# Kernel optimization log

Measured on AMD Instinct MI355X. Metric: run time of the kernel, lower is better.

## Reference

```python
import math
import jax, jax.numpy as jnp
import numpy as np

B, C, H, W = 8, 512, 32, 32
N_HEADS = 8
N_GROUPS = 32  # GroupNorm(32) as in guided-diffusion normalization()
EPS = 1e-5


def setup_inputs() -> dict:
    key = jax.random.key(0)
    k0, k1, k2, k3, k4 = jax.random.split(key, 5)
    x = jax.random.normal(k0, (B, C, H, W), dtype=jnp.float32)
    gn_scale = jnp.ones((C,), dtype=jnp.float32)
    gn_bias = jnp.zeros((C,), dtype=jnp.float32)
    # 1x1 conv weights stored as (out, in); proj_out is zero-initialized in the
    # original but we use small random weights so the op is non-trivial.
    qkv_w = jax.random.normal(k1, (3 * C, C), dtype=jnp.float32) * 0.02
    qkv_b = jax.random.normal(k2, (3 * C,), dtype=jnp.float32) * 0.02
    proj_w = jax.random.normal(k3, (C, C), dtype=jnp.float32) * 0.02
    proj_b = jax.random.normal(k4, (C,), dtype=jnp.float32) * 0.02
    return {"x": x, "gn_scale": gn_scale, "gn_bias": gn_bias,
            "qkv_w": qkv_w, "qkv_b": qkv_b, "proj_w": proj_w, "proj_b": proj_b}


def reference(x, gn_scale, gn_bias, qkv_w, qkv_b, proj_w, proj_b):
    b, c, h, w = x.shape
    L = h * w
    xf = x.reshape(b, c, L)

    # GroupNorm(32): normalize over (channels-in-group, length)
    xg = xf.reshape(b, N_GROUPS, c // N_GROUPS, L)
    mu = jnp.mean(xg, axis=(2, 3), keepdims=True)
    var = jnp.var(xg, axis=(2, 3), keepdims=True)
    xn = ((xg - mu) * jax.lax.rsqrt(var + EPS)).reshape(b, c, L)
    xn = xn * gn_scale[None, :, None] + gn_bias[None, :, None]

    # 1x1 conv -> qkv (b, 3c, L)
    qkv = jnp.einsum('oc,bcl->bol', qkv_w, xn) + qkv_b[None, :, None]

    ch = c // N_HEADS  # head dim (width//(3*n_heads) of qkv)
    q, k, v = jnp.split(qkv, 3, axis=1)
    q = q.reshape(b * N_HEADS, ch, L)
    k = k.reshape(b * N_HEADS, ch, L)
    v = v.reshape(b * N_HEADS, ch, L)

    scale = 1.0 / math.sqrt(math.sqrt(ch))
    # scores: (b*heads, L, L) materialized, as in the original
    wts = jnp.einsum('bct,bcs->bts', q * scale, k * scale)
    wts = jax.nn.softmax(wts.astype(jnp.float32), axis=-1).astype(q.dtype)
    a = jnp.einsum('bts,bcs->bct', wts, v).reshape(b, c, L)

    # zero-initialized 1x1 proj in original; random weights here
    hout = jnp.einsum('oc,bcl->bol', proj_w, a) + proj_b[None, :, None]
    return (xf + hout).reshape(b, c, h, w)
```

## Files before the change

kernel.cpp:

```cpp
#include <hip/hip_runtime.h>
#include <math.h>

#define BATCH   8
#define CCH     512
#define LL      1024
#define NHEADS  8
#define CHD     64
#define EPSV    1e-5f
#define QSCALE  0.1803368801111204f

typedef __bf16 bf16_t;
typedef bf16_t bf16x8 __attribute__((ext_vector_type(8)));
typedef bf16_t bf16x4 __attribute__((ext_vector_type(4)));
typedef float  f32x4  __attribute__((ext_vector_type(4)));

__device__ __forceinline__ bf16_t f2b(float f) {
  unsigned u = __float_as_uint(f);
  u += 0x7fff + ((u >> 16) & 1);
  return __builtin_bit_cast(bf16_t, (unsigned short)(u >> 16));
}

__device__ __forceinline__ unsigned pack2(float lo, float hi) {
  unsigned a = (unsigned)__builtin_bit_cast(unsigned short, f2b(lo));
  unsigned b = (unsigned)__builtin_bit_cast(unsigned short, f2b(hi));
  return (b << 16) | a;
}

__device__ __forceinline__ void gload_lds16(const void* g, void* l) {
  __builtin_amdgcn_global_load_lds(
      (const __attribute__((address_space(1))) void*)g,
      (__attribute__((address_space(3))) void*)l, 16, 0, 0);
}

__global__ __launch_bounds__(256) void prep_fused(const float* __restrict__ qkvw,
                                                  const float* __restrict__ projw,
                                                  bf16_t* __restrict__ wqb,
                                                  bf16_t* __restrict__ wpb,
                                                  const float* __restrict__ x,
                                                  const float* __restrict__ gsc,
                                                  const float* __restrict__ gbi,
                                                  bf16_t* __restrict__ xnT) {
  int bid = blockIdx.x;
  int tid = threadIdx.x;
  if (bid < 1024) {
    int i = (bid * 256 + tid) * 4;
    const float* src;
    bf16_t* dst;
    int j;
    if (i < 1536 * 512) { src = qkvw; dst = wqb; j = i; }
    else                { src = projw; dst = wpb; j = i - 1536 * 512; }
    float4 v = *(const float4*)(src + j);
    bf16x4 o = {f2b(v.x), f2b(v.y), f2b(v.z), f2b(v.w)};
    *(bf16x4*)(dst + j) = o;
    return;
  }
  int lin = bid - 1024;
  int xcd = lin & 7, slot = lin >> 3;
  int b = slot & 7, jj = slot >> 3;
  int g = xcd * 4 + jj;
  const float4* x4 = (const float4*)(x + ((size_t)(b * 32 + g)) * 16 * LL);

  float s = 0.f, ss = 0.f;
  float4 v[16];
#pragma unroll
  for (int it = 0; it < 16; ++it) {
    float4 f = x4[it * 256 + tid];
    v[it] = f;
    s += f.x + f.y + f.z + f.w;
    ss += f.x * f.x + f.y * f.y + f.z * f.z + f.w * f.w;
  }
#pragma unroll
  for (int m = 1; m < 64; m <<= 1) { s += __shfl_xor(s, m); ss += __shfl_xor(ss, m); }
  __shared__ float rs_[4], rss[4];
  int wv = tid >> 6, ln = tid & 63;
  if (ln == 0) { rs_[wv] = s; rss[wv] = ss; }
  __syncthreads();
  s  = rs_[0] + rs_[1] + rs_[2] + rs_[3];
  ss = rss[0] + rss[1] + rss[2] + rss[3];
  float mean = s * (1.f / 16384.f);
  float var  = ss * (1.f / 16384.f) - mean * mean;
  float rstd = rsqrtf(var + EPSV);

  float sc[16], bi[16];
#pragma unroll
  for (int it = 0; it < 16; ++it) {
    sc[it] = gsc[g * 16 + it] * rstd;
    bi[it] = gbi[g * 16 + it] - mean * sc[it];
  }

#pragma unroll
  for (int j = 0; j < 4; ++j) {
    unsigned w[8];
#pragma unroll
    for (int k = 0; k < 8; ++k) {
      float a0 = (j == 0 ? v[2 * k].x : j == 1 ? v[2 * k].y : j == 2 ? v[2 * k].z : v[2 * k].w);
      float a1 = (j == 0 ? v[2 * k + 1].x : j == 1 ? v[2 * k + 1].y : j == 2 ? v[2 * k + 1].z : v[2 * k + 1].w);
      w[k] = pack2(a0 * sc[2 * k] + bi[2 * k], a1 * sc[2 * k + 1] + bi[2 * k + 1]);
    }
    int l = tid * 4 + j;
    bf16_t* dst = xnT + ((size_t)b * LL + l) * CCH + g * 16;
    *(uint4*)dst = make_uint4(w[0], w[1], w[2], w[3]);
    *(uint4*)(dst + 8) = make_uint4(w[4], w[5], w[6], w[7]);
  }
}

__global__ __launch_bounds__(256, 3) void qkv_mfma(const bf16_t* __restrict__ wq,
                                                   const bf16_t* __restrict__ xnT,
                                                   const float* __restrict__ qkvb,
                                                   bf16_t* __restrict__ qt,
                                                   bf16_t* __restrict__ kt,
                                                   bf16_t* __restrict__ vt) {
  __shared__ bf16_t As[128 * 64];
  __shared__ bf16_t Bs[2][128 * 64];
  int tid = threadIdx.x;
  int wave = tid >> 6, lane = tid & 63;
  int lrow = lane & 15, quad = lane >> 4;
  int wm = wave >> 1, wn = wave & 1;
  int b = blockIdx.x;
  int oBase = blockIdx.y * 128, lBase = blockIdx.z * 128;
  int srow = lane >> 3;
  int sgOff = (((lane & 7) ^ srow) << 4);

#pragma unroll
  for (int j = 0; j < 4; ++j) {
    int ci = wave * 4 + j;
    int R = ci * 8 + srow;
    gload_lds16((const char*)(xnT + ((size_t)b * LL + lBase + R) * CCH) + sgOff,
                (char*)&Bs[0][0] + ci * 1024);
  }

  f32x4 acc[4][4] = {};
  for (int ktile = 0; ktile < 8; ++ktile) {
    int cur = ktile & 1;
    int kB = ktile * 64;
    __builtin_amdgcn_sched_barrier(0);
    __builtin_amdgcn_s_barrier();
    __builtin_amdgcn_sched_barrier(0);
#pragma unroll
    for (int j = 0; j < 4; ++j) {
      int ci = wave * 4 + j;
      int R = ci * 8 + srow;
      gload_lds16((const char*)(wq + (size_t)(oBase + R) * CCH + kB) + sgOff,
                  (char*)As + ci * 1024);
    }
    if (ktile < 7) {
#pragma unroll
      for (int j = 0; j < 4; ++j) {
        int ci = wave * 4 + j;
        int R = ci * 8 + srow;
        gload_lds16((const char*)(xnT + ((size_t)b * LL + lBase + R) * CCH + kB + 64) + sgOff,
                    (char*)&Bs[cur ^ 1][0] + ci * 1024);
      }
      asm volatile("s_waitcnt vmcnt(4)" ::: "memory");
    } else {
      asm volatile("s_waitcnt vmcnt(0)" ::: "memory");
    }
    __builtin_amdgcn_s_barrier();
    __builtin_amdgcn_sched_barrier(0);
    const bf16_t* bsrc = &Bs[cur][0];
#pragma unroll
    for (int kk = 0; kk < 2; ++kk) {
      int g = (kk * 4 + quad) ^ (lrow & 7);
      bf16x8 af[4], bfr[4];
#pragma unroll
      for (int m = 0; m < 4; ++m) {
        int r = wm * 64 + m * 16 + lrow;
        af[m] = *(const bf16x8*)(As + r * 64 + g * 8);
      }
#pragma unroll
      for (int n = 0; n < 4; ++n) {
        int r = wn * 64 + n * 16 + lrow;
        bfr[n] = *(const bf16x8*)(bsrc + r * 64 + g * 8);
      }
#pragma unroll
      for (int m = 0; m < 4; ++m)
#pragma unroll
        for (int n = 0; n < 4; ++n)
          acc[m][n] = __builtin_amdgcn_mfma_f32_16x16x32_bf16(af[m], bfr[n], acc[m][n], 0, 0, 0);
    }
  }

  int oW = oBase + wm * 64;
  int lW = lBase + wn * 64;
  int sec = oW >> 9;
#pragma unroll
  for (int m = 0; m < 4; ++m) {
    int o4 = oW + m * 16 + quad * 4;
    float4 bb4 = *(const float4*)&qkvb[o4];
    int cc = o4 & 511;
    int head = cc >> 6, ch = cc & 63;
    int bh = b * NHEADS + head;
    if (sec == 0) {
#pragma unroll
      for (int n = 0; n < 4; ++n) {
        int l = lW + n * 16 + lrow;
        unsigned d0 = pack2((acc[m][n][0] + bb4.x) * QSCALE,
                            (acc[m][n][1] + bb4.y) * QSCALE);
        unsigned d1 = pack2((acc[m][n][2] + bb4.z) * QSCALE,
                            (acc[m][n][3] + bb4.w) * QSCALE);
        *(uint2*)(qt + ((size_t)bh * LL + l) * CHD + ch) = make_uint2(d0, d1);
      }
    } else if (sec == 1) {
#pragma unroll
      for (int n = 0; n < 4; ++n) {
        int l = lW + n * 16 + lrow;
        unsigned d0 = pack2(acc[m][n][0] + bb4.x, acc[m][n][1] + bb4.y);
        unsigned d1 = pack2(acc[m][n][2] + bb4.z, acc[m][n][3] + bb4.w);
        *(uint2*)(kt + ((size_t)bh * LL + l) * CHD + ch) = make_uint2(d0, d1);
      }
    } else {
      float bb[4] = {bb4.x, bb4.y, bb4.z, bb4.w};
#pragma unroll
      for (int i = 0; i < 4; ++i) {
        unsigned d0 = pack2(acc[m][0][i] + bb[i], acc[m][1][i] + bb[i]);
        unsigned d1 = pack2(acc[m][2][i] + bb[i], acc[m][3][i] + bb[i]);
        *(uint2*)(vt + ((size_t)bh * CHD + ch + i) * LL + lW + lrow * 4) =
            make_uint2(d0, d1);
      }
    }
  }
}

__global__ __launch_bounds__(256) void attn_mfma(const bf16_t* __restrict__ qt,
                                                 const bf16_t* __restrict__ kt,
                                                 const bf16_t* __restrict__ vt,
                                                 bf16_t* __restrict__ at) {
  __shared__ bf16_t kbuf[2][64 * 64];
  __shared__ bf16_t vbuf[2][64 * 64];
  __shared__ bf16_t pb[8 * 16 * 72];
  int tid = threadIdx.x, wave = tid >> 6, lane = tid & 63;
  int lrow = lane & 15, quad = lane >> 4;
  int bh = blockIdx.x;
  int tW = blockIdx.y * 128 + wave * 32;
  const bf16_t* qb = qt + (size_t)bh * LL * CHD;
  const bf16_t* kb = kt + (size_t)bh * LL * CHD;
  const bf16_t* vb = vt + (size_t)bh * CHD * LL;

  int srow = lane >> 3;
  int sgb = (((lane & 7) ^ srow) << 4);

  bf16x8 qf[2][2];
#pragma unroll
  for (int h = 0; h < 2; ++h) {
    const bf16_t* qp = qb + (size_t)(tW + h * 16 + lrow) * CHD + quad * 8;
    qf[h][0] = *(const bf16x8*)qp;
    qf[h][1] = *(const bf16x8*)(qp + 32);
  }

  bf16x8 ones;
#pragma unroll
  for (int j = 0; j < 8; ++j) ones[j] = (bf16_t)1.0f;

  f32x4 Oa[2][4] = {};
  f32x4 Os[2] = {};

#pragma unroll
  for (int j = 0; j < 2; ++j) {
    int c = wave * 2 + j;
    int R = c * 8 + srow;
    gload_lds16((const char*)(kb + (size_t)R * CHD) + sgb, (char*)&kbuf[0][0] + c * 1024);
    gload_lds16((const char*)(vb + (size_t)R * LL) + sgb, (char*)&vbuf[0][0] + c * 1024);
  }
  __syncthreads();

  int swz0 = (quad ^ (lrow & 7)) * 8;
  int swz1 = ((quad + 4) ^ (lrow & 7)) * 8;

  for (int st = 0; st < 16; ++st) {
    int cur = st & 1;
    if (st < 15) {
      int sBn = (st + 1) * 64;
#pragma unroll
      for (int j = 0; j < 2; ++j) {
        int c = wave * 2 + j;
        int R = c * 8 + srow;
        gload_lds16((const char*)(kb + (size_t)(sBn + R) * CHD) + sgb,
                    (char*)&kbuf[cur ^ 1][0] + c * 1024);
        gload_lds16((const char*)(vb + (size_t)R * LL + sBn) + sgb,
                    (char*)&vbuf[cur ^ 1][0] + c * 1024);
      }
    }
    const bf16_t* kbase = &kbuf[cur][0];
    const bf16_t* vbase = &vbuf[cur][0];

    f32x4 S[2][4];
    __builtin_amdgcn_s_setprio(1);
#pragma unroll
    for (int ss = 0; ss < 4; ++ss) {
      int s = ss * 16 + lrow;
      bf16x8 k0 = *(const bf16x8*)(kbase + s * 64 + swz0);
      bf16x8 k1 = *(const bf16x8*)(kbase + s * 64 + swz1);
#pragma unroll
      for (int h = 0; h < 2; ++h) {
        f32x4 z = {0.f, 0.f, 0.f, 0.f};
        z = __builtin_amdgcn_mfma_f32_16x16x32_bf16(qf[h][0], k0, z, 0, 0, 0);
        S[h][ss] = __builtin_amdgcn_mfma_f32_16x16x32_bf16(qf[h][1], k1, z, 0, 0, 0);
      }
    }
    __builtin_amdgcn_s_setprio(0);

#pragma unroll
    for (int h = 0; h < 2; ++h) {
      bf16_t* pw = pb + (wave * 2 + h) * (16 * 72);
      float p[4][4];
#pragma unroll
      for (int ss = 0; ss < 4; ++ss)
#pragma unroll
        for (int i = 0; i < 4; ++i)
          p[ss][i] = __builtin_amdgcn_exp2f(S[h][ss][i]);
#pragma unroll
      for (int i = 0; i < 4; ++i) {
        unsigned d0 = __builtin_amdgcn_perm(__float_as_uint(p[1][i]),
                                            __float_as_uint(p[0][i]), 0x07060302u);
        unsigned d1 = __builtin_amdgcn_perm(__float_as_uint(p[3][i]),
                                            __float_as_uint(p[2][i]), 0x07060302u);
        uint2* dst = (uint2*)(pw + (quad * 4 + i) * 72 + lrow * 4);
        *dst = make_uint2(d0, d1);
      }
    }
    asm volatile("s_waitcnt lgkmcnt(0)" ::: "memory");

    bf16x8 pf[2][2];
#pragma unroll
    for (int h = 0; h < 2; ++h) {
      const bf16_t* pw = pb + (wave * 2 + h) * (16 * 72);
      pf[h][0] = *(const bf16x8*)(pw + lrow * 72 + quad * 8);
      pf[h][1] = *(const bf16x8*)(pw + lrow * 72 + 32 + quad * 8);
    }

    __builtin_amdgcn_s_setprio(1);
#pragma unroll
    for (int n = 0; n < 4; ++n) {
      int r = (n * 16 + lrow) * 64;
      bf16x8 v0 = *(const bf16x8*)(vbase + r + swz0);
      bf16x8 v1 = *(const bf16x8*)(vbase + r + swz1);
#pragma unroll
      for (int h = 0; h < 2; ++h) {
        Oa[h][n] = __builtin_amdgcn_mfma_f32_16x16x32_bf16(pf[h][0], v0, Oa[h][n], 0, 0, 0);
        Oa[h][n] = __builtin_amdgcn_mfma_f32_16x16x32_bf16(pf[h][1], v1, Oa[h][n], 0, 0, 0);
      }
    }
#pragma unroll
    for (int h = 0; h < 2; ++h) {
      Os[h] = __builtin_amdgcn_mfma_f32_16x16x32_bf16(pf[h][0], ones, Os[h], 0, 0, 0);
      Os[h] = __builtin_amdgcn_mfma_f32_16x16x32_bf16(pf[h][1], ones, Os[h], 0, 0, 0);
    }
    __builtin_amdgcn_s_setprio(0);

    __syncthreads();
  }

  bf16_t* ab = at + (size_t)bh * LL * CHD;
#pragma unroll
  for (int h = 0; h < 2; ++h) {
    float inv[4];
#pragma unroll
    for (int i = 0; i < 4; ++i) inv[i] = 1.f / Os[h][i];
#pragma unroll
    for (int n = 0; n < 4; ++n)
#pragma unroll
      for (int i = 0; i < 4; ++i)
        ab[(size_t)(tW + h * 16 + quad * 4 + i) * CHD + n * 16 + lrow] =
            f2b(Oa[h][n][i] * inv[i]);
  }
}

__global__ __launch_bounds__(256) void proj_mfma(const bf16_t* __restrict__ wp,
                                                 const bf16_t* __restrict__ at,
                                                 const float* __restrict__ projb,
                                                 const float* __restrict__ x,
                                                 float* __restrict__ out) {
  __shared__ bf16_t As[2][128 * 64];
  __shared__ bf16_t Bs[2][64 * 64];
  int tid = threadIdx.x;
  int wave = tid >> 6, lane = tid & 63;
  int lrow = lane & 15, quad = lane >> 4;
  int wm = wave >> 1, wn = wave & 1;
  int b = blockIdx.x;
  int oBase = blockIdx.y * 128, lBase = blockIdx.z * 64;
  int srow = lane >> 3;
  int sgOff = (((lane & 7) ^ srow) << 4);

  auto stage = [&](int buf, int ktile) {
    int kB = ktile * 64;
#pragma unroll
    for (int j = 0; j < 4; ++j) {
      int ci = wave * 4 + j;
      int R = ci * 8 + srow;
      gload_lds16((const char*)(wp + (size_t)(oBase + R) * CCH + kB) + sgOff,
                  (char*)&As[buf][0] + ci * 1024);
    }
#pragma unroll
    for (int j = 0; j < 2; ++j) {
      int ci = wave * 2 + j;
      int R = ci * 8 + srow;
      gload_lds16((const char*)(at + ((size_t)(b * NHEADS + ktile) * LL + lBase + R) * CHD) + sgOff,
                  (char*)&Bs[buf][0] + ci * 1024);
    }
  };

  stage(0, 0);
  __syncthreads();

  f32x4 acc[4][2] = {};
  for (int ktile = 0; ktile < 8; ++ktile) {
    int cur = ktile & 1;
    if (ktile < 7) stage(cur ^ 1, ktile + 1);
    const bf16_t* asrc = &As[cur][0];
    const bf16_t* bsrc = &Bs[cur][0];
#pragma unroll
    for (int kk = 0; kk < 2; ++kk) {
      int g = (kk * 4 + quad) ^ (lrow & 7);
      bf16x8 af[4], bfr[2];
#pragma unroll
      for (int m = 0; m < 4; ++m) {
        int r = wm * 64 + m * 16 + lrow;
        af[m] = *(const bf16x8*)(asrc + r * 64 + g * 8);
      }
#pragma unroll
      for (int n = 0; n < 2; ++n) {
        int r = wn * 32 + n * 16 + lrow;
        bfr[n] = *(const bf16x8*)(bsrc + r * 64 + g * 8);
      }
#pragma unroll
      for (int m = 0; m < 4; ++m)
#pragma unroll
        for (int n = 0; n < 2; ++n)
          acc[m][n] = __builtin_amdgcn_mfma_f32_16x16x32_bf16(af[m], bfr[n], acc[m][n], 0, 0, 0);
    }
    if (ktile < 7) __syncthreads();
  }

  int oW = oBase + wm * 64;
  int lW = lBase + wn * 32;
#pragma unroll
  for (int m = 0; m < 4; ++m) {
#pragma unroll
    for (int i = 0; i < 4; ++i) {
      int o = oW + m * 16 + quad * 4 + i;
      float bb = projb[o];
#pragma unroll
      for (int n = 0; n < 2; ++n) {
        int l = lW + n * 16 + lrow;
        size_t off = ((size_t)(b * CCH + o)) * LL + l;
        out[off] = acc[m][n][i] + bb + x[off];
      }
    }
  }
}

extern "C" void kernel_launch(void* const* d_in, const int* in_sizes, int n_in,
                              void* d_out, int out_size, void* d_ws, size_t ws_size,
                              hipStream_t stream) {
  const float* x     = (const float*)d_in[0];
  const float* gsc   = (const float*)d_in[1];
  const float* gbi   = (const float*)d_in[2];
  const float* qkvw  = (const float*)d_in[3];
  const float* qkvb  = (const float*)d_in[4];
  const float* projw = (const float*)d_in[5];
  const float* projb = (const float*)d_in[6];
  float* out = (float*)d_out;

  char* ws = (char*)d_ws;
  bf16_t* wqb   = (bf16_t*)(ws + 4096);
  bf16_t* wpb   = (bf16_t*)(ws + 4096 + 1572864);
  bf16_t* xnT   = (bf16_t*)(ws + 2101248);
  bf16_t* qt    = (bf16_t*)(ws + 2101248 + 8388608);
  bf16_t* kt    = (bf16_t*)(ws + 2101248 + 2 * 8388608);
  bf16_t* vt    = (bf16_t*)(ws + 2101248 + 3 * 8388608);
  bf16_t* at    = (bf16_t*)(ws + 2101248 + 4 * 8388608);

  hipLaunchKernelGGL(prep_fused, dim3(1280), dim3(256), 0, stream,
                     qkvw, projw, wqb, wpb, x, gsc, gbi, xnT);
  hipLaunchKernelGGL(qkv_mfma, dim3(BATCH, 12, 8), dim3(256), 0, stream,
                     wqb, xnT, qkvb, qt, kt, vt);
  hipLaunchKernelGGL(attn_mfma, dim3(64, 8), dim3(256), 0, stream, qt, kt, vt, at);
  hipLaunchKernelGGL(proj_mfma, dim3(BATCH, 4, 16), dim3(256), 0, stream,
                     wpb, at, projb, x, out);
}
```

Measured before the change: 142.4 us.

## Keep softmax probabilities in registers and compute row sums in VALU

The attention kernel now computes S transposed (K as the A operand), so each lane's exp'd probabilities line up directly with the B-operand layout of a 16x16x16 bf16 MFMA. The P tile no longer round-trips through LDS. The row sum is accumulated with VALU adds plus two cross-lane shuffles, replacing the extra MFMAs against a ones vector. Packing uses the hardware v_cvt_pk_bf16_f32 instruction, and launch bounds request 3 blocks per CU. In exchange it issues more, smaller MFMAs and narrower V loads from LDS, and the V-write in the QKV kernel becomes scalar 2-byte stores.

Result: no change. 144.2 us (+1.2%).

```diff
diff --git a/kernel.cpp b/kernel.cpp
--- a/kernel.cpp
+++ b/kernel.cpp
@@ -13,6 +13,7 @@
 typedef bf16_t bf16x8 __attribute__((ext_vector_type(8)));
 typedef bf16_t bf16x4 __attribute__((ext_vector_type(4)));
 typedef float  f32x4  __attribute__((ext_vector_type(4)));
+typedef short  s16x4  __attribute__((ext_vector_type(4)));
 
 __device__ __forceinline__ bf16_t f2b(float f) {
   unsigned u = __float_as_uint(f);
@@ -24,6 +25,12 @@
   unsigned a = (unsigned)__builtin_bit_cast(unsigned short, f2b(lo));
   unsigned b = (unsigned)__builtin_bit_cast(unsigned short, f2b(hi));
   return (b << 16) | a;
+}
+
+__device__ __forceinline__ unsigned cvtpk_bf16(float lo, float hi) {
+  unsigned r;
+  asm("v_cvt_pk_bf16_f32 %0, %1, %2" : "=v"(r) : "v"(lo), "v"(hi));
+  return r;
 }
 
 __device__ __forceinline__ void gload_lds16(const void* g, void* l) {
@@ -212,22 +219,21 @@
       float bb[4] = {bb4.x, bb4.y, bb4.z, bb4.w};
 #pragma unroll
       for (int i = 0; i < 4; ++i) {
-        unsigned d0 = pack2(acc[m][0][i] + bb[i], acc[m][1][i] + bb[i]);
-        unsigned d1 = pack2(acc[m][2][i] + bb[i], acc[m][3][i] + bb[i]);
-        *(uint2*)(vt + ((size_t)bh * CHD + ch + i) * LL + lW + lrow * 4) =
-            make_uint2(d0, d1);
-      }
-    }
-  }
-}
-
-__global__ __launch_bounds__(256) void attn_mfma(const bf16_t* __restrict__ qt,
-                                                 const bf16_t* __restrict__ kt,
-                                                 const bf16_t* __restrict__ vt,
-                                                 bf16_t* __restrict__ at) {
+        bf16_t* vrow = vt + ((size_t)bh * CHD + ch + i) * LL;
+#pragma unroll
+        for (int n = 0; n < 4; ++n)
+          vrow[lW + n * 16 + lrow] = f2b(acc[m][n][i] + bb[i]);
+      }
+    }
+  }
+}
+
+__global__ __launch_bounds__(256, 3) void attn_mfma(const bf16_t* __restrict__ qt,
+                                                    const bf16_t* __restrict__ kt,
+                                                    const bf16_t* __restrict__ vt,
+                                                    bf16_t* __restrict__ at) {
   __shared__ bf16_t kbuf[2][64 * 64];
   __shared__ bf16_t vbuf[2][64 * 64];
-  __shared__ bf16_t pb[8 * 16 * 72];
   int tid = threadIdx.x, wave = tid >> 6, lane = tid & 63;
   int lrow = lane & 15, quad = lane >> 4;
   int bh = blockIdx.x;
@@ -247,12 +253,8 @@
     qf[h][1] = *(const bf16x8*)(qp + 32);
   }
 
-  bf16x8 ones;
-#pragma unroll
-  for (int j = 0; j < 8; ++j) ones[j] = (bf16_t)1.0f;
-
   f32x4 Oa[2][4] = {};
-  f32x4 Os[2] = {};
+  float Osum[2] = {0.f, 0.f};
 
 #pragma unroll
   for (int j = 0; j < 2; ++j) {
@@ -293,75 +295,63 @@
 #pragma unroll
       for (int h = 0; h < 2; ++h) {
         f32x4 z = {0.f, 0.f, 0.f, 0.f};
-        z = __builtin_amdgcn_mfma_f32_16x16x32_bf16(qf[h][0], k0, z, 0, 0, 0);
-        S[h][ss] = __builtin_amdgcn_mfma_f32_16x16x32_bf16(qf[h][1], k1, z, 0, 0, 0);
+        z = __builtin_amdgcn_mfma_f32_16x16x32_bf16(k0, qf[h][0], z, 0, 0, 0);
+        S[h][ss] = __builtin_amdgcn_mfma_f32_16x16x32_bf16(k1, qf[h][1], z, 0, 0, 0);
       }
     }
     __builtin_amdgcn_s_setprio(0);
 
-#pragma unroll
-    for (int h = 0; h < 2; ++h) {
-      bf16_t* pw = pb + (wave * 2 + h) * (16 * 72);
-      float p[4][4];
-#pragma unroll
-      for (int ss = 0; ss < 4; ++ss)
-#pragma unroll
-        for (int i = 0; i < 4; ++i)
-          p[ss][i] = __builtin_amdgcn_exp2f(S[h][ss][i]);
-#pragma unroll
-      for (int i = 0; i < 4; ++i) {
-        unsigned d0 = __builtin_amdgcn_perm(__float_as_uint(p[1][i]),
-                                            __float_as_uint(p[0][i]), 0x07060302u);
-        unsigned d1 = __builtin_amdgcn_perm(__float_as_uint(p[3][i]),
-                                            __float_as_uint(p[2][i]), 0x07060302u);
-        uint2* dst = (uint2*)(pw + (quad * 4 + i) * 72 + lrow * 4);
-        *dst = make_uint2(d0, d1);
-      }
-    }
-    asm volatile("s_waitcnt lgkmcnt(0)" ::: "memory");
-
-    bf16x8 pf[2][2];
-#pragma unroll
-    for (int h = 0; h < 2; ++h) {
-      const bf16_t* pw = pb + (wave * 2 + h) * (16 * 72);
-      pf[h][0] = *(const bf16x8*)(pw + lrow * 72 + quad * 8);
-      pf[h][1] = *(const bf16x8*)(pw + lrow * 72 + 32 + quad * 8);
-    }
+    s16x4 pf[2][4];
+#pragma unroll
+    for (int h = 0; h < 2; ++h)
+#pragma unroll
+      for (int ss = 0; ss < 4; ++ss) {
+        float p0 = __builtin_amdgcn_exp2f(S[h][ss][0]);
+        float p1 = __builtin_amdgcn_exp2f(S[h][ss][1]);
+        float p2 = __builtin_amdgcn_exp2f(S[h][ss][2]);
+        float p3 = __builtin_amdgcn_exp2f(S[h][ss][3]);
+        Osum[h] += (p0 + p1) + (p2 + p3);
+        unsigned u0 = cvtpk_bf16(p0, p1);
+        unsigned u1 = cvtpk_bf16(p2, p3);
+        unsigned long long uu = ((unsigned long long)u1 << 32) | u0;
+        pf[h][ss] = __builtin_bit_cast(s16x4, uu);
+      }
 
     __builtin_amdgcn_s_setprio(1);
 #pragma unroll
     for (int n = 0; n < 4; ++n) {
-      int r = (n * 16 + lrow) * 64;
-      bf16x8 v0 = *(const bf16x8*)(vbase + r + swz0);
-      bf16x8 v1 = *(const bf16x8*)(vbase + r + swz1);
-#pragma unroll
-      for (int h = 0; h < 2; ++h) {
-        Oa[h][n] = __builtin_amdgcn_mfma_f32_16x16x32_bf16(pf[h][0], v0, Oa[h][n], 0, 0, 0);
-        Oa[h][n] = __builtin_amdgcn_mfma_f32_16x16x32_bf16(pf[h][1], v1, Oa[h][n], 0, 0, 0);
-      }
-    }
-#pragma unroll
-    for (int h = 0; h < 2; ++h) {
-      Os[h] = __builtin_amdgcn_mfma_f32_16x16x32_bf16(pf[h][0], ones, Os[h], 0, 0, 0);
-      Os[h] = __builtin_amdgcn_mfma_f32_16x16x32_bf16(pf[h][1], ones, Os[h], 0, 0, 0);
+      int rv = n * 16 + lrow;
+#pragma unroll
+      for (int ss = 0; ss < 4; ++ss) {
+        int slot = ((ss << 1) + (quad >> 1)) ^ (lrow & 7);
+        s16x4 vfrag = *(const s16x4*)(vbase + rv * 64 + slot * 8 + (quad & 1) * 4);
+#pragma unroll
+        for (int h = 0; h < 2; ++h)
+          Oa[h][n] = __builtin_amdgcn_mfma_f32_16x16x16bf16_1k(vfrag, pf[h][ss], Oa[h][n], 0, 0, 0);
+      }
     }
     __builtin_amdgcn_s_setprio(0);
 
     __syncthreads();
   }
 
+#pragma unroll
+  for (int h = 0; h < 2; ++h) {
+    Osum[h] += __shfl_xor(Osum[h], 16);
+    Osum[h] += __shfl_xor(Osum[h], 32);
+  }
+
   bf16_t* ab = at + (size_t)bh * LL * CHD;
 #pragma unroll
   for (int h = 0; h < 2; ++h) {
-    float inv[4];
-#pragma unroll
-    for (int i = 0; i < 4; ++i) inv[i] = 1.f / Os[h][i];
-#pragma unroll
-    for (int n = 0; n < 4; ++n)
-#pragma unroll
-      for (int i = 0; i < 4; ++i)
-        ab[(size_t)(tW + h * 16 + quad * 4 + i) * CHD + n * 16 + lrow] =
-            f2b(Oa[h][n][i] * inv[i]);
+    float inv = 1.f / Osum[h];
+    int row = tW + h * 16 + lrow;
+#pragma unroll
+    for (int n = 0; n < 4; ++n) {
+      unsigned d0 = pack2(Oa[h][n][0] * inv, Oa[h][n][1] * inv);
+      unsigned d1 = pack2(Oa[h][n][2] * inv, Oa[h][n][3] * inv);
+      *(uint2*)(ab + (size_t)row * CHD + n * 16 + quad * 4) = make_uint2(d0, d1);
+    }
   }
 }
 
```

## Triple-buffer K/V and GEMM tiles with vmcnt-based partial waits

Applied to the files above, without the earlier changes.

Moves the attention and projection kernels from double to triple buffering in LDS, issuing loads two tiles ahead. The full __syncthreads is replaced by an explicit s_waitcnt vmcnt(N) that waits only for the older tile, followed by s_barrier and sched_barrier fences. The goal is to hide more global-load latency behind MFMA work. In exchange the kernels use more shared memory per block, which may reduce occupancy, especially in the projection kernel.

Measured after the change: 140.1 us (median of 3 runs). Within noise of the previous version (-1.6%).

```diff
diff --git a/kernel.cpp b/kernel.cpp
--- a/kernel.cpp
+++ b/kernel.cpp
@@ -225,8 +225,8 @@
                                                  const bf16_t* __restrict__ kt,
                                                  const bf16_t* __restrict__ vt,
                                                  bf16_t* __restrict__ at) {
-  __shared__ bf16_t kbuf[2][64 * 64];
-  __shared__ bf16_t vbuf[2][64 * 64];
+  __shared__ bf16_t kbuf[3][64 * 64];
+  __shared__ bf16_t vbuf[3][64 * 64];
   __shared__ bf16_t pb[8 * 16 * 72];
   int tid = threadIdx.x, wave = tid >> 6, lane = tid & 63;
   int lrow = lane & 15, quad = lane >> 4;
@@ -239,6 +239,19 @@
   int srow = lane >> 3;
   int sgb = (((lane & 7) ^ srow) << 4);
 
+  auto stageKV = [&](int buf, int tile) {
+    int sBn = tile * 64;
+#pragma unroll
+    for (int j = 0; j < 2; ++j) {
+      int c = wave * 2 + j;
+      int R = c * 8 + srow;
+      gload_lds16((const char*)(kb + (size_t)(sBn + R) * CHD) + sgb,
+                  (char*)&kbuf[buf][0] + c * 1024);
+      gload_lds16((const char*)(vb + (size_t)R * LL + sBn) + sgb,
+                  (char*)&vbuf[buf][0] + c * 1024);
+    }
+  };
+
   bf16x8 qf[2][2];
 #pragma unroll
   for (int h = 0; h < 2; ++h) {
@@ -254,32 +267,19 @@
   f32x4 Oa[2][4] = {};
   f32x4 Os[2] = {};
 
-#pragma unroll
-  for (int j = 0; j < 2; ++j) {
-    int c = wave * 2 + j;
-    int R = c * 8 + srow;
-    gload_lds16((const char*)(kb + (size_t)R * CHD) + sgb, (char*)&kbuf[0][0] + c * 1024);
-    gload_lds16((const char*)(vb + (size_t)R * LL) + sgb, (char*)&vbuf[0][0] + c * 1024);
-  }
-  __syncthreads();
+  stageKV(0, 0);
+  stageKV(1, 1);
+  __builtin_amdgcn_sched_barrier(0);
+  asm volatile("s_waitcnt vmcnt(4)" ::: "memory");
+  __builtin_amdgcn_s_barrier();
+  __builtin_amdgcn_sched_barrier(0);
 
   int swz0 = (quad ^ (lrow & 7)) * 8;
   int swz1 = ((quad + 4) ^ (lrow & 7)) * 8;
 
   for (int st = 0; st < 16; ++st) {
-    int cur = st & 1;
-    if (st < 15) {
-      int sBn = (st + 1) * 64;
-#pragma unroll
-      for (int j = 0; j < 2; ++j) {
-        int c = wave * 2 + j;
-        int R = c * 8 + srow;
-        gload_lds16((const char*)(kb + (size_t)(sBn + R) * CHD) + sgb,
-                    (char*)&kbuf[cur ^ 1][0] + c * 1024);
-        gload_lds16((const char*)(vb + (size_t)R * LL + sBn) + sgb,
-                    (char*)&vbuf[cur ^ 1][0] + c * 1024);
-      }
-    }
+    int cur = st % 3;
+    if (st + 2 < 16) stageKV((st + 2) % 3, st + 2);
     const bf16_t* kbase = &kbuf[cur][0];
     const bf16_t* vbase = &vbuf[cur][0];
 
@@ -347,7 +347,16 @@
     }
     __builtin_amdgcn_s_setprio(0);
 
-    __syncthreads();
+    if (st < 15) {
+      __builtin_amdgcn_sched_barrier(0);
+      if (st + 2 < 16) {
+        asm volatile("s_waitcnt vmcnt(4)" ::: "memory");
+      } else {
+        asm volatile("s_waitcnt vmcnt(0)" ::: "memory");
+      }
+      __builtin_amdgcn_s_barrier();
+      __builtin_amdgcn_sched_barrier(0);
+    }
   }
 
   bf16_t* ab = at + (size_t)bh * LL * CHD;
@@ -370,8 +379,8 @@
                                                  const float* __restrict__ projb,
                                                  const float* __restrict__ x,
                                                  float* __restrict__ out) {
-  __shared__ bf16_t As[2][128 * 64];
-  __shared__ bf16_t Bs[2][64 * 64];
+  __shared__ bf16_t As[3][128 * 64];
+  __shared__ bf16_t Bs[3][64 * 64];
   int tid = threadIdx.x;
   int wave = tid >> 6, lane = tid & 63;
   int lrow = lane & 15, quad = lane >> 4;
@@ -400,12 +409,16 @@
   };
 
   stage(0, 0);
-  __syncthreads();
+  stage(1, 1);
+  __builtin_amdgcn_sched_barrier(0);
+  asm volatile("s_waitcnt vmcnt(6)" ::: "memory");
+  __builtin_amdgcn_s_barrier();
+  __builtin_amdgcn_sched_barrier(0);
 
   f32x4 acc[4][2] = {};
   for (int ktile = 0; ktile < 8; ++ktile) {
-    int cur = ktile & 1;
-    if (ktile < 7) stage(cur ^ 1, ktile + 1);
+    int cur = ktile % 3;
+    if (ktile + 2 < 8) stage((ktile + 2) % 3, ktile + 2);
     const bf16_t* asrc = &As[cur][0];
     const bf16_t* bsrc = &Bs[cur][0];
 #pragma unroll
@@ -428,7 +441,16 @@
         for (int n = 0; n < 2; ++n)
           acc[m][n] = __builtin_amdgcn_mfma_f32_16x16x32_bf16(af[m], bfr[n], acc[m][n], 0, 0, 0);
     }
-    if (ktile < 7) __syncthreads();
+    if (ktile < 7) {
+      __builtin_amdgcn_sched_barrier(0);
+      if (ktile + 2 < 8) {
+        asm volatile("s_waitcnt vmcnt(6)" ::: "memory");
+      } else {
+        asm volatile("s_waitcnt vmcnt(0)" ::: "memory");
+      }
+      __builtin_amdgcn_s_barrier();
+      __builtin_amdgcn_sched_barrier(0);
+    }
   }
 
   int oW = oBase + wm * 64;
```
